# Kernel tuning notes

Measured on AMD Instinct MI355X. Metric: run time of the kernel, lower is better.

The kernel has to match this reference:

```python
import jax, jax.numpy as jnp
import numpy as np

A, R = 180, 180  # numAngle, numRho
EPS = 1e-5


def _hough_seg_ids(H, W):
    # Deep Hough Transform binning (Hanqer/deep-hough-transform initTab):
    # irho = int(sqrt(H^2+W^2)+1)/(numRho-1); theta_k = k*pi/numAngle
    irho = int(np.sqrt(H * H + W * W) + 1) / float(R - 1)
    theta = np.arange(A) * (np.pi / A)
    tab_cos = np.cos(theta) / irho  # [A]
    tab_sin = np.sin(theta) / irho
    xs = np.arange(W) - W // 2  # x is width index
    ys = np.arange(H) - H // 2
    r = np.round(tab_cos[:, None, None] * xs[None, None, :]
                 + tab_sin[:, None, None] * ys[None, :, None]).astype(np.int64) + R // 2
    r = np.clip(r, 0, R - 1)
    return jnp.asarray(r.reshape(A, H * W))  # [A, H*W] rho-bin per (angle, pixel)


def _conv_bn_relu(x, w, b, g, beta, m, v, pad):
    y = jax.lax.conv_general_dilated(
        x, w, window_strides=(1, 1), padding=[(pad, pad), (pad, pad)],
        dimension_numbers=('NCHW', 'OIHW', 'NCHW'))
    y = y + b[None, :, None, None]
    scale = g / jnp.sqrt(v + EPS)
    y = (y - m[None, :, None, None]) * scale[None, :, None, None] + beta[None, :, None, None]
    return jax.nn.relu(y)


def _dht(f):
    # f: [N, C, H, W] -> accum [N, C, A, R]
    N, C, H, W = f.shape
    seg = _hough_seg_ids(H, W)  # [A, HW]
    ft = f.reshape(N, C, H * W).transpose(2, 0, 1).reshape(H * W, N * C)  # [HW, N*C]
    acc = jax.vmap(lambda s: jax.ops.segment_sum(ft, s, num_segments=R))(seg)  # [A, R, N*C]
    return acc.reshape(A, R, N, C).transpose(2, 3, 0, 1)  # [N, C, A, R]


def setup_inputs() -> dict:
    key = jax.random.key(0)
    ks = jax.random.split(key, 24)
    N, Ci, dim, H, W = 8, 256, 128, 128, 128
    inp = {
        'x': jax.random.normal(ks[0], (N, Ci, H, W), jnp.float32),
        'w1': jax.random.normal(ks[1], (dim, Ci, 1, 1), jnp.float32) * (1.0 / np.sqrt(Ci)),
        'b1': jax.random.normal(ks[2], (dim,), jnp.float32) * 0.01,
        'g1': jax.random.uniform(ks[3], (dim,), jnp.float32, 0.5, 1.5),
        'be1': jax.random.normal(ks[4], (dim,), jnp.float32) * 0.01,
        'm1': jax.random.normal(ks[5], (dim,), jnp.float32) * 0.1,
        'v1': jax.random.uniform(ks[6], (dim,), jnp.float32, 0.5, 1.5),
        'w2': jax.random.normal(ks[7], (dim, dim, 3, 3), jnp.float32) * (1.0 / np.sqrt(dim * 9)),
        'b2': jax.random.normal(ks[8], (dim,), jnp.float32) * 0.01,
        'g2': jax.random.uniform(ks[9], (dim,), jnp.float32, 0.5, 1.5),
        'be2': jax.random.normal(ks[10], (dim,), jnp.float32) * 0.01,
        'm2': jax.random.normal(ks[11], (dim,), jnp.float32) * 0.1,
        'v2': jax.random.uniform(ks[12], (dim,), jnp.float32, 0.5, 1.5),
        'w3': jax.random.normal(ks[13], (dim, dim, 3, 3), jnp.float32) * (1.0 / np.sqrt(dim * 9)),
        'b3': jax.random.normal(ks[14], (dim,), jnp.float32) * 0.01,
        'g3': jax.random.uniform(ks[15], (dim,), jnp.float32, 0.5, 1.5),
        'be3': jax.random.normal(ks[16], (dim,), jnp.float32) * 0.01,
        'm3': jax.random.normal(ks[17], (dim,), jnp.float32) * 0.1,
        'v3': jax.random.uniform(ks[18], (dim,), jnp.float32, 0.5, 1.5),
    }
    return inp


def reference(x, w1, b1, g1, be1, m1, v1,
              w2, b2, g2, be2, m2, v2,
              w3, b3, g3, be3, m3, v3):
    f = _conv_bn_relu(x, w1, b1, g1, be1, m1, v1, pad=0)   # 1x1 conv + BN + ReLU
    acc = _dht(f)                                           # [N, dim, A, R]
    y = _conv_bn_relu(acc, w2, b2, g2, be2, m2, v2, pad=1)  # 3x3 conv + BN + ReLU
    y = _conv_bn_relu(y, w3, b3, g3, be3, m3, v3, pad=1)
    return y
```

## Files before the change

### kernel.cpp

```cpp
#include <hip/hip_runtime.h>
#include <hip/hip_bf16.h>
#include <math.h>

#define NB 8
#define CI 256
#define CD 128
#define HH 128
#define WW 128
#define HW (HH*WW)
#define AANG 180
#define RRHO 180
#define PADD 182
#define M2 (AANG*RRHO)

typedef __attribute__((ext_vector_type(8))) short short8;
typedef __attribute__((ext_vector_type(8))) _Float16 half8;
typedef __attribute__((ext_vector_type(2))) _Float16 h2;
typedef __attribute__((ext_vector_type(4))) float floatx4;
typedef __attribute__((ext_vector_type(2))) float floatx2;

static __device__ __forceinline__ void async_cp16(const void* g, void* l) {
  __builtin_amdgcn_global_load_lds((const __attribute__((address_space(1))) unsigned int*)g,
                                   (__attribute__((address_space(3))) unsigned int*)l,
                                   16, 0, 0);
}

static __device__ __forceinline__ unsigned short f2bf(float f) {
  unsigned int u = __builtin_bit_cast(unsigned int, f);
  unsigned int r = (u + 0x7fffu + ((u >> 16) & 1u)) >> 16;
  return (unsigned short)r;
}

static __device__ __forceinline__ unsigned short f2h(float f) {
  return __builtin_bit_cast(unsigned short, (_Float16)f);
}

static __device__ __forceinline__ void acc2(float& aL, float& aH, unsigned int u,
                                            h2 eL, h2 eH) {
  h2 hv = __builtin_bit_cast(h2, u);
#if __has_builtin(__builtin_amdgcn_fdot2)
  aL = __builtin_amdgcn_fdot2(hv, eL, aL, false);
  aH = __builtin_amdgcn_fdot2(hv, eH, aH, false);
#else
  aL += (float)hv.x;
  aH += (float)hv.y;
#endif
}

static __device__ __forceinline__ void acc4(float* aL, float* aH, const uint4& v,
                                            h2 eL, h2 eH) {
  acc2(aL[0], aH[0], v.x, eL, eH);
  acc2(aL[1], aH[1], v.y, eL, eH);
  acc2(aL[2], aH[2], v.z, eL, eH);
  acc2(aL[3], aH[3], v.w, eL, eH);
}

__global__ void prep_kernel(const float* __restrict__ w1, const float* __restrict__ w2,
                            const float* __restrict__ w3,
                            const float* b1, const float* g1, const float* be1,
                            const float* m1, const float* v1,
                            const float* b2, const float* g2, const float* be2,
                            const float* m2, const float* v2,
                            const float* b3, const float* g3, const float* be3,
                            const float* m3, const float* v3,
                            unsigned short* __restrict__ wK1, unsigned short* __restrict__ wK2,
                            unsigned short* __restrict__ wK3,
                            float* __restrict__ sc, float* __restrict__ sh) {
  int idx = blockIdx.x * 256 + threadIdx.x;
  if (idx < 32768) {
    wK1[idx] = f2h(w1[idx]);
  } else if (idx < 32768 + 147456) {
    int i = idx - 32768;
    int co = i / 1152, k = i % 1152;
    int dydx = k >> 7, ci = k & 127;
    int dst = (((dydx*2 + (ci >> 6)) * 128 + co) * 64) + (ci & 63);
    wK2[dst] = f2bf(w2[(size_t)(co*128 + ci)*9 + dydx]);
  } else if (idx < 32768 + 2*147456) {
    int i = idx - 32768 - 147456;
    int co = i / 1152, k = i % 1152;
    int dydx = k >> 7, ci = k & 127;
    int dst = (((dydx*2 + (ci >> 6)) * 128 + co) * 64) + (ci & 63);
    wK3[dst] = f2bf(w3[(size_t)(co*128 + ci)*9 + dydx]);
  } else if (idx < 32768 + 2*147456 + 384) {
    int j = idx - 32768 - 2*147456;
    int c = j >> 7, co = j & 127;
    const float* b  = c==0?b1 :(c==1?b2 :b3);
    const float* g  = c==0?g1 :(c==1?g2 :g3);
    const float* be = c==0?be1:(c==1?be2:be3);
    const float* m  = c==0?m1 :(c==1?m2 :m3);
    const float* v  = c==0?v1 :(c==1?v2 :v3);
    float s = g[co] * rsqrtf(v[co] + 1e-5f);
    sc[c*128 + co] = s;
    sh[c*128 + co] = (b[co] - m[co]) * s + be[co];
  }
}

__global__ void hist_kernel(unsigned char* __restrict__ seg, unsigned int* __restrict__ offs) {
  int a = blockIdx.x, t = threadIdx.x;
  __shared__ unsigned int h[RRHO];
  if (t < RRHO) h[t] = 0;
  __syncthreads();
  double th = (double)a * (M_PI / 180.0);
  double Cc = cos(th) / (182.0 / 179.0);
  double Ss = sin(th) / (182.0 / 179.0);
  for (int p = t; p < HW; p += 256) {
    int x = (p & 127) - 64;
    int y = (p >> 7) - 64;
    int r = (int)rint(Cc * (double)x + Ss * (double)y) + 90;
    r = r < 0 ? 0 : (r > 179 ? 179 : r);
    seg[(size_t)a*HW + p] = (unsigned char)r;
    atomicAdd(&h[r], 1u);
  }
  __syncthreads();
  if (t == 0) {
    unsigned int run = 0;
    for (int r = 0; r < RRHO; ++r) { offs[a*192 + r] = run; run += h[r]; }
    offs[a*192 + RRHO] = run;
  }
}

__global__ void fill_kernel(const unsigned char* __restrict__ seg,
                            const unsigned int* __restrict__ offs,
                            unsigned short* __restrict__ lst16) {
  int a = blockIdx.x, t = threadIdx.x;
  __shared__ unsigned int pos[RRHO];
  if (t < RRHO) pos[t] = offs[a*192 + t];
  __syncthreads();
  int p0 = t * 64;
  for (int i = 0; i < 64; ++i) {
    int p = p0 + i;
    int r = seg[(size_t)a*HW + p];
    unsigned int ix = atomicAdd(&pos[r], 1u);
    lst16[(size_t)a*HW + ix] = (unsigned short)p;
  }
}

__global__ void zero_border(uint4* __restrict__ accP, uint4* __restrict__ y2P,
                            unsigned int* __restrict__ qcnt) {
  int idx = blockIdx.x * 256 + threadIdx.x;
  if (idx < 8) qcnt[idx] = 0;
  if (idx >= NB * PADD * PADD) return;
  int rc = idx % (PADD * PADD);
  int row = rc / PADD, col = rc % PADD;
  if (row != 0 && row != PADD-1 && col != 0 && col != PADD-1) return;
  uint4 z = {0u, 0u, 0u, 0u};
  size_t base = (size_t)idx * 16;
  #pragma unroll
  for (int i = 0; i < 16; ++i) { accP[base + i] = z; y2P[base + i] = z; }
}

__global__ __launch_bounds__(256) void conv1_kernel(
    const float* __restrict__ x, const unsigned short* __restrict__ wK,
    const float* __restrict__ sc, const float* __restrict__ sh,
    unsigned short* __restrict__ f) {
  __shared__ short Al[4*128*8];
  __shared__ short Bl[4*128*8];
  int t = threadIdx.x;
  int m0 = blockIdx.x * 128;
  int n = blockIdx.y;
  int lane = t & 63, wv = t >> 6, wm = wv & 1, wn = wv >> 1;
  int mloc = t & 127, octb = t >> 7;
  floatx4 acc[4][4];
  #pragma unroll
  for (int i = 0; i < 4; ++i)
    #pragma unroll
    for (int j = 0; j < 4; ++j) acc[i][j] = (floatx4){0.f, 0.f, 0.f, 0.f};
  const float* xn = x + (size_t)n * CI * HW;
  for (int kc = 0; kc < 8; ++kc) {
    if (kc) __syncthreads();
    #pragma unroll
    for (int j = 0; j < 2; ++j) {
      int oct = octb + 2*j;
      const float* src = xn + (size_t)(kc*32 + oct*8) * HW + m0 + mloc;
      float v[8];
      #pragma unroll
      for (int e = 0; e < 8; ++e) v[e] = src[(size_t)e * HW];
      uint4 pk;
      pk.x = __builtin_bit_cast(unsigned int, __builtin_amdgcn_cvt_pkrtz(v[0], v[1]));
      pk.y = __builtin_bit_cast(unsigned int, __builtin_amdgcn_cvt_pkrtz(v[2], v[3]));
      pk.z = __builtin_bit_cast(unsigned int, __builtin_amdgcn_cvt_pkrtz(v[4], v[5]));
      pk.w = __builtin_bit_cast(unsigned int, __builtin_amdgcn_cvt_pkrtz(v[6], v[7]));
      *reinterpret_cast<uint4*>(&Al[(size_t)(t + 256*j) * 8]) = pk;
    }
    #pragma unroll
    for (int j = 0; j < 2; ++j) {
      int oct = octb + 2*j;
      async_cp16(wK + (size_t)mloc * 256 + kc*32 + oct*8,
                 &Bl[(size_t)((t & 0xFFC0) + 256*j) * 8]);
    }
    __syncthreads();
    int q = lane >> 4, l15 = lane & 15;
    short8 af[4], bfr[4];
    #pragma unroll
    for (int i = 0; i < 4; ++i)
      af[i] = *reinterpret_cast<const short8*>(&Al[((q*128) + wm*64 + i*16 + l15) * 8]);
    #pragma unroll
    for (int j = 0; j < 4; ++j)
      bfr[j] = *reinterpret_cast<const short8*>(&Bl[((q*128) + wn*64 + j*16 + l15) * 8]);
    #pragma unroll
    for (int i = 0; i < 4; ++i)
      #pragma unroll
      for (int j = 0; j < 4; ++j)
        acc[i][j] = __builtin_amdgcn_mfma_f32_16x16x32_f16(
            __builtin_bit_cast(half8, af[i]), __builtin_bit_cast(half8, bfr[j]),
            acc[i][j], 0, 0, 0);
  }
  int q = lane >> 4, l15 = lane & 15;
  #pragma unroll
  for (int j = 0; j < 4; ++j) {
    int co = wn*64 + j*16 + l15;
    float s = sc[co], hb = sh[co];
    #pragma unroll
    for (int i = 0; i < 4; ++i) {
      #pragma unroll
      for (int rg = 0; rg < 4; ++rg) {
        int m = m0 + wm*64 + i*16 + q*4 + rg;
        float v = acc[i][j][rg] * s + hb;
        v = fmaxf(v, 0.f);
        f[((size_t)n * HW + m) * 128 + co] = f2h(v);
      }
    }
  }
}

__global__ __launch_bounds__(512, 8) void dht_kernel(
    const unsigned short* __restrict__ lst16, const unsigned int* __restrict__ offs,
    const unsigned int* __restrict__ f, unsigned int* __restrict__ accP,
    unsigned int* __restrict__ qcnt) {
  __shared__ unsigned short Ls[HW];
  __shared__ unsigned int Os[RRHO + 1];
  __shared__ int sWork;
  int t = threadIdx.x;
  if (t == 0) {
    unsigned int xcd;
    asm volatile("s_getreg_b32 %0, hwreg(HW_REG_XCC_ID, 0, 32)" : "=s"(xcd));
    xcd &= 7u;
    int work = 0;
    for (int k = 0; k < 8; ++k) {
      unsigned int q = (xcd + (unsigned int)k) & 7u;
      unsigned int tk = atomicAdd(&qcnt[q], 1u);
      if (tk < 360u) { work = (int)(q * 360u + tk); break; }
    }
    sWork = work;
  }
  __syncthreads();
  int work = sWork;
  int n = work / 360;
  int rem = work % 360;
  int h = rem / 180;
  int a = rem % 180;
  {
    const uint4* src = (const uint4*)(lst16 + (size_t)a * HW);
    uint4* dst = (uint4*)Ls;
    if (t < RRHO + 1) Os[t] = offs[a*192 + t];
    #pragma unroll
    for (int i = 0; i < 4; ++i) dst[t + 512*i] = src[t + 512*i];
  }
  __syncthreads();
  int w = t >> 6, lane = t & 63;
  int sub = lane >> 3;
  int co  = lane & 7;
  const char* fb = (const char*)(f + (size_t)n * HW * 64);
  unsigned int loff = (unsigned int)(h*32 + co*4) * 4u;
  const h2 eL = {(_Float16)1.0f, (_Float16)0.0f};
  const h2 eH = {(_Float16)0.0f, (_Float16)1.0f};
  for (int r = w; r < RRHO; r += 8) {
    int lo = (int)Os[r];
    int hi = (int)Os[r+1];
    float accL[4], accH[4];
    #pragma unroll
    for (int j = 0; j < 4; ++j) { accL[j] = 0.f; accH[j] = 0.f; }
    while (hi - lo >= 64) {
      unsigned int p0 = Ls[lo + sub];
      unsigned int p1 = Ls[lo + 8 + sub];
      unsigned int p2 = Ls[lo + 16 + sub];
      unsigned int p3 = Ls[lo + 24 + sub];
      unsigned int p4 = Ls[hi - 32 + sub];
      unsigned int p5 = Ls[hi - 24 + sub];
      unsigned int p6 = Ls[hi - 16 + sub];
      unsigned int p7 = Ls[hi - 8 + sub];
      uint4 v0 = *(const uint4*)(fb + ((p0 << 8) + loff));
      uint4 v1 = *(const uint4*)(fb + ((p1 << 8) + loff));
      uint4 v2 = *(const uint4*)(fb + ((p2 << 8) + loff));
      uint4 v3 = *(const uint4*)(fb + ((p3 << 8) + loff));
      uint4 v4 = *(const uint4*)(fb + ((p4 << 8) + loff));
      uint4 v5 = *(const uint4*)(fb + ((p5 << 8) + loff));
      uint4 v6 = *(const uint4*)(fb + ((p6 << 8) + loff));
      uint4 v7 = *(const uint4*)(fb + ((p7 << 8) + loff));
      acc4(accL, accH, v0, eL, eH); acc4(accL, accH, v1, eL, eH);
      acc4(accL, accH, v2, eL, eH); acc4(accL, accH, v3, eL, eH);
      acc4(accL, accH, v4, eL, eH); acc4(accL, accH, v5, eL, eH);
      acc4(accL, accH, v6, eL, eH); acc4(accL, accH, v7, eL, eH);
      lo += 32; hi -= 32;
    }
    for (; lo + 32 <= hi; lo += 32) {
      unsigned int p0 = Ls[lo + sub];
      unsigned int p1 = Ls[lo + 8 + sub];
      unsigned int p2 = Ls[lo + 16 + sub];
      unsigned int p3 = Ls[lo + 24 + sub];
      uint4 v0 = *(const uint4*)(fb + ((p0 << 8) + loff));
      uint4 v1 = *(const uint4*)(fb + ((p1 << 8) + loff));
      uint4 v2 = *(const uint4*)(fb + ((p2 << 8) + loff));
      uint4 v3 = *(const uint4*)(fb + ((p3 << 8) + loff));
      acc4(accL, accH, v0, eL, eH); acc4(accL, accH, v1, eL, eH);
      acc4(accL, accH, v2, eL, eH); acc4(accL, accH, v3, eL, eH);
    }
    for (; lo + 8 <= hi; lo += 8) {
      unsigned int p0 = Ls[lo + sub];
      uint4 v0 = *(const uint4*)(fb + ((p0 << 8) + loff));
      acc4(accL, accH, v0, eL, eH);
    }
    if (lo < hi) {
      int idx = lo + sub;
      int cl = idx < hi ? idx : (hi - 1);
      unsigned int p0 = Ls[cl];
      uint4 v0 = *(const uint4*)(fb + ((p0 << 8) + loff));
      if (idx >= hi) { v0.x = 0; v0.y = 0; v0.z = 0; v0.w = 0; }
      acc4(accL, accH, v0, eL, eH);
    }
    #pragma unroll
    for (int m = 8; m <= 32; m <<= 1) {
      #pragma unroll
      for (int j = 0; j < 4; ++j) {
        accL[j] += __shfl_xor(accL[j], m, 64);
        accH[j] += __shfl_xor(accH[j], m, 64);
      }
    }
    if (sub == 0) {
      uint4 out;
      out.x = (unsigned int)f2bf(accL[0]) | ((unsigned int)f2bf(accH[0]) << 16);
      out.y = (unsigned int)f2bf(accL[1]) | ((unsigned int)f2bf(accH[1]) << 16);
      out.z = (unsigned int)f2bf(accL[2]) | ((unsigned int)f2bf(accH[2]) << 16);
      out.w = (unsigned int)f2bf(accL[3]) | ((unsigned int)f2bf(accH[3]) << 16);
      size_t o = (((size_t)n*PADD + (a+1))*PADD + (r+1))*64 + h*32 + co*4;
      *(uint4*)(accP + o) = out;
    }
  }
}

template<int MODE>
__global__ __launch_bounds__(256) void conv3x3_kernel(
    const unsigned short* __restrict__ inP,
    const unsigned short* __restrict__ wKr,
    const float* __restrict__ sc, const float* __restrict__ sh,
    void* __restrict__ outp) {
  __shared__ short Al[2][128*64];
  __shared__ short Bl[2][128*64];
  int t = threadIdx.x;
  int m0 = blockIdx.x * 128;
  int n = blockIdx.y;
  int lane = t & 63, w = t >> 6, wm = w & 1, wn = w >> 1;
  floatx4 acc[4][4];
  #pragma unroll
  for (int i = 0; i < 4; ++i)
    #pragma unroll
    for (int j = 0; j < 4; ++j) acc[i][j] = (floatx4){0.f, 0.f, 0.f, 0.f};

  int srcOct = ((lane & 7) - (lane >> 3)) & 7;
  const unsigned short* rpA[4];
  unsigned int offB[4];
  #pragma unroll
  for (int i = 0; i < 4; ++i) {
    int row = w*32 + i*8 + (lane >> 3);
    int mg = m0 + row; if (mg > M2 - 1) mg = M2 - 1;
    int oa = mg / 180, orr = mg % 180;
    rpA[i] = inP + (((size_t)n*PADD + oa)*PADD + orr)*128 + srcOct*8;
    offB[i] = (unsigned int)(row*64 + srcOct*8);
  }

  auto stage = [&](int step, int b) {
    int dydx = step >> 1, cc2 = step & 1;
    int dy = (dydx * 11) >> 5, dx = dydx - dy*3;
    int doff = (dy*PADD + dx)*128 + cc2*64;
    #pragma unroll
    for (int i = 0; i < 4; ++i) {
      async_cp16(rpA[i] + doff, &Al[b][(size_t)((w*4 + i)*64 + lane) * 8]);
      async_cp16(wKr + (size_t)step*8192 + offB[i],
                 &Bl[b][(size_t)((w*4 + i)*64 + lane) * 8]);
    }
  };
  auto compute = [&](int b) {
    int q = lane >> 4, l15 = lane & 15;
    #pragma unroll
    for (int kk = 0; kk < 2; ++kk) {
      int o = kk*4 + q;
      int swz = ((o + l15) & 7) * 8;
      short8 rf[4], cf[4];
      #pragma unroll
      for (int i = 0; i < 4; ++i) {
        int addr = (wm*64 + i*16 + l15)*64 + swz;
        rf[i] = *reinterpret_cast<const short8*>(MODE == 1 ? &Al[b][addr] : &Bl[b][addr]);
      }
      #pragma unroll
      for (int j = 0; j < 4; ++j) {
        int addr = (wn*64 + j*16 + l15)*64 + swz;
        cf[j] = *reinterpret_cast<const short8*>(MODE == 1 ? &Bl[b][addr] : &Al[b][addr]);
      }
      #pragma unroll
      for (int i = 0; i < 4; ++i)
        #pragma unroll
        for (int j = 0; j < 4; ++j)
          acc[i][j] = __builtin_amdgcn_mfma_f32_16x16x32_bf16(rf[i], cf[j], acc[i][j], 0, 0, 0);
    }
  };

  stage(0, 0);
  #pragma unroll 1
  for (int s2 = 0; s2 < 9; ++s2) {
    stage(2*s2 + 1, 1);
    asm volatile("s_waitcnt vmcnt(8)" ::: "memory");
    __builtin_amdgcn_s_barrier();
    __builtin_amdgcn_sched_barrier(0);
    compute(0);
    asm volatile("s_waitcnt lgkmcnt(0)" ::: "memory");
    __builtin_amdgcn_s_barrier();
    if (s2 < 8) {
      stage(2*s2 + 2, 0);
      asm volatile("s_waitcnt vmcnt(8)" ::: "memory");
    } else {
      asm volatile("s_waitcnt vmcnt(0)" ::: "memory");
    }
    __builtin_amdgcn_s_barrier();
    __builtin_amdgcn_sched_barrier(0);
    compute(1);
    asm volatile("s_waitcnt lgkmcnt(0)" ::: "memory");
    __builtin_amdgcn_s_barrier();
  }

  int q = lane >> 4, l15 = lane & 15;
  if (MODE == 1) {
    unsigned short* out = (unsigned short*)outp;
    #pragma unroll
    for (int j = 0; j < 4; ++j) {
      int co = wn*64 + j*16 + l15;
      float s = sc[co], hb = sh[co];
      #pragma unroll
      for (int i = 0; i < 4; ++i) {
        #pragma unroll
        for (int rg = 0; rg < 4; ++rg) {
          int m = m0 + wm*64 + i*16 + q*4 + rg;
          if (m < M2) {
            float v = fmaxf(acc[i][j][rg] * s + hb, 0.f);
            int oa2 = m / 180, or2 = m % 180;
            out[(((size_t)n*PADD + oa2 + 1)*PADD + or2 + 1)*128 + co] = f2bf(v);
          }
        }
      }
    }
  } else {
    float* out = (float*)outp;
    #pragma unroll
    for (int i = 0; i < 4; ++i) {
      #pragma unroll
      for (int rg = 0; rg < 4; ++rg) {
        int co = wm*64 + i*16 + q*4 + rg;
        float s = sc[co], hb = sh[co];
        #pragma unroll
        for (int j = 0; j < 4; ++j) {
          int m = m0 + wn*64 + j*16 + l15;
          if (m < M2) {
            float v = fmaxf(acc[i][j][rg] * s + hb, 0.f);
            out[((size_t)n*128 + co)*M2 + m] = v;
          }
        }
      }
    }
  }
}

extern "C" void kernel_launch(void* const* d_in, const int* in_sizes, int n_in,
                              void* d_out, int out_size, void* d_ws, size_t ws_size,
                              hipStream_t stream) {
  const float* x  = (const float*)d_in[0];
  const float* w1 = (const float*)d_in[1];
  const float* b1 = (const float*)d_in[2];
  const float* g1 = (const float*)d_in[3];
  const float* be1= (const float*)d_in[4];
  const float* m1 = (const float*)d_in[5];
  const float* v1 = (const float*)d_in[6];
  const float* w2 = (const float*)d_in[7];
  const float* b2 = (const float*)d_in[8];
  const float* g2 = (const float*)d_in[9];
  const float* be2= (const float*)d_in[10];
  const float* m2 = (const float*)d_in[11];
  const float* v2 = (const float*)d_in[12];
  const float* w3 = (const float*)d_in[13];
  const float* b3 = (const float*)d_in[14];
  const float* g3 = (const float*)d_in[15];
  const float* be3= (const float*)d_in[16];
  const float* m3 = (const float*)d_in[17];
  const float* v3 = (const float*)d_in[18];

  size_t off = 0;
  char* ws = (char*)d_ws;
  auto alloc = [&](size_t sz) -> void* {
    void* p = ws + off;
    off = (off + sz + 255) & ~(size_t)255;
    return p;
  };
  unsigned short* fbuf = (unsigned short*)alloc((size_t)NB*HW*128*2);
  unsigned short* accP = (unsigned short*)alloc((size_t)NB*PADD*PADD*128*2);
  unsigned short* y2P  = (unsigned short*)alloc((size_t)NB*PADD*PADD*128*2);
  unsigned short* wK1  = (unsigned short*)alloc(32768*2);
  unsigned short* wK2  = (unsigned short*)alloc(147456*2);
  unsigned short* wK3  = (unsigned short*)alloc(147456*2);
  float* sc = (float*)alloc(384*4);
  float* sh = (float*)alloc(384*4);
  unsigned char* seg  = (unsigned char*)alloc((size_t)AANG*HW);
  unsigned int* offs  = (unsigned int*)alloc((size_t)AANG*192*4);
  unsigned short* lst16 = (unsigned short*)alloc((size_t)AANG*HW*2);
  unsigned int* qcnt  = (unsigned int*)alloc(8*4);

  prep_kernel<<<1282, 256, 0, stream>>>(w1, w2, w3,
      b1, g1, be1, m1, v1, b2, g2, be2, m2, v2, b3, g3, be3, m3, v3,
      wK1, wK2, wK3, sc, sh);
  hist_kernel<<<AANG, 256, 0, stream>>>(seg, offs);
  fill_kernel<<<AANG, 256, 0, stream>>>(seg, offs, lst16);
  zero_border<<<(NB*PADD*PADD + 255)/256, 256, 0, stream>>>((uint4*)accP, (uint4*)y2P, qcnt);
  conv1_kernel<<<dim3(HW/128, NB), 256, 0, stream>>>(x, wK1, sc, sh, fbuf);
  dht_kernel<<<NB*AANG*2, 512, 0, stream>>>(lst16, offs, (const unsigned int*)fbuf,
                                            (unsigned int*)accP, qcnt);
  conv3x3_kernel<1><<<dim3((M2 + 127)/128, NB), 256, 0, stream>>>(
      accP, wK2, sc + 128, sh + 128, y2P);
  conv3x3_kernel<2><<<dim3((M2 + 127)/128, NB), 256, 0, stream>>>(
      y2P, wK3, sc + 256, sh + 256, d_out);
}
```

Before: 790.8 us.

## Fuse hist/fill kernels and single-buffer conv3x3 with higher occupancy

Merges the Hough histogram and list-fill kernels into one kernel that keeps rho-bin ids in shared memory, removing a launch and the global seg buffer. The conv3x3 kernel drops its hand-scheduled double-buffered async pipeline in favour of a single LDS buffer with plain __syncthreads and a min-blocks launch bound of 4. This aims for more resident blocks to hide latency, but it gives up the explicit overlap of loads with MFMA compute.

```diff
diff --git a/kernel.cpp b/kernel.cpp
--- a/kernel.cpp
+++ b/kernel.cpp
@@ -95,9 +95,12 @@
   }
 }
 
-__global__ void hist_kernel(unsigned char* __restrict__ seg, unsigned int* __restrict__ offs) {
+__global__ void histfill_kernel(unsigned int* __restrict__ offs,
+                                unsigned short* __restrict__ lst16) {
   int a = blockIdx.x, t = threadIdx.x;
+  __shared__ unsigned char segL[HW];
   __shared__ unsigned int h[RRHO];
+  __shared__ unsigned int pos[RRHO];
   if (t < RRHO) h[t] = 0;
   __syncthreads();
   double th = (double)a * (M_PI / 180.0);
@@ -108,28 +111,24 @@
     int y = (p >> 7) - 64;
     int r = (int)rint(Cc * (double)x + Ss * (double)y) + 90;
     r = r < 0 ? 0 : (r > 179 ? 179 : r);
-    seg[(size_t)a*HW + p] = (unsigned char)r;
+    segL[p] = (unsigned char)r;
     atomicAdd(&h[r], 1u);
   }
   __syncthreads();
   if (t == 0) {
     unsigned int run = 0;
-    for (int r = 0; r < RRHO; ++r) { offs[a*192 + r] = run; run += h[r]; }
+    for (int r = 0; r < RRHO; ++r) {
+      pos[r] = run;
+      offs[a*192 + r] = run;
+      run += h[r];
+    }
     offs[a*192 + RRHO] = run;
   }
-}
-
-__global__ void fill_kernel(const unsigned char* __restrict__ seg,
-                            const unsigned int* __restrict__ offs,
-                            unsigned short* __restrict__ lst16) {
-  int a = blockIdx.x, t = threadIdx.x;
-  __shared__ unsigned int pos[RRHO];
-  if (t < RRHO) pos[t] = offs[a*192 + t];
   __syncthreads();
   int p0 = t * 64;
   for (int i = 0; i < 64; ++i) {
     int p = p0 + i;
-    int r = seg[(size_t)a*HW + p];
+    int r = segL[p];
     unsigned int ix = atomicAdd(&pos[r], 1u);
     lst16[(size_t)a*HW + ix] = (unsigned short)p;
   }
@@ -339,13 +338,13 @@
 }
 
 template<int MODE>
-__global__ __launch_bounds__(256) void conv3x3_kernel(
+__global__ __launch_bounds__(256, 4) void conv3x3_kernel(
     const unsigned short* __restrict__ inP,
     const unsigned short* __restrict__ wKr,
     const float* __restrict__ sc, const float* __restrict__ sh,
     void* __restrict__ outp) {
-  __shared__ short Al[2][128*64];
-  __shared__ short Bl[2][128*64];
+  __shared__ short Al[128*64];
+  __shared__ short Bl[128*64];
   int t = threadIdx.x;
   int m0 = blockIdx.x * 128;
   int n = blockIdx.y;
@@ -368,18 +367,18 @@
     offB[i] = (unsigned int)(row*64 + srcOct*8);
   }
 
-  auto stage = [&](int step, int b) {
+  for (int step = 0; step < 18; ++step) {
     int dydx = step >> 1, cc2 = step & 1;
     int dy = (dydx * 11) >> 5, dx = dydx - dy*3;
     int doff = (dy*PADD + dx)*128 + cc2*64;
+    if (step) __syncthreads();
     #pragma unroll
     for (int i = 0; i < 4; ++i) {
-      async_cp16(rpA[i] + doff, &Al[b][(size_t)((w*4 + i)*64 + lane) * 8]);
+      async_cp16(rpA[i] + doff, &Al[(size_t)((w*4 + i)*64 + lane) * 8]);
       async_cp16(wKr + (size_t)step*8192 + offB[i],
-                 &Bl[b][(size_t)((w*4 + i)*64 + lane) * 8]);
-    }
-  };
-  auto compute = [&](int b) {
+                 &Bl[(size_t)((w*4 + i)*64 + lane) * 8]);
+    }
+    __syncthreads();
     int q = lane >> 4, l15 = lane & 15;
     #pragma unroll
     for (int kk = 0; kk < 2; ++kk) {
@@ -389,12 +388,12 @@
       #pragma unroll
       for (int i = 0; i < 4; ++i) {
         int addr = (wm*64 + i*16 + l15)*64 + swz;
-        rf[i] = *reinterpret_cast<const short8*>(MODE == 1 ? &Al[b][addr] : &Bl[b][addr]);
+        rf[i] = *reinterpret_cast<const short8*>(MODE == 1 ? &Al[addr] : &Bl[addr]);
       }
       #pragma unroll
       for (int j = 0; j < 4; ++j) {
         int addr = (wn*64 + j*16 + l15)*64 + swz;
-        cf[j] = *reinterpret_cast<const short8*>(MODE == 1 ? &Bl[b][addr] : &Al[b][addr]);
+        cf[j] = *reinterpret_cast<const short8*>(MODE == 1 ? &Bl[addr] : &Al[addr]);
       }
       #pragma unroll
       for (int i = 0; i < 4; ++i)
@@ -402,31 +401,7 @@
         for (int j = 0; j < 4; ++j)
           acc[i][j] = __builtin_amdgcn_mfma_f32_16x16x32_bf16(rf[i], cf[j], acc[i][j], 0, 0, 0);
     }
-  };
-
-  stage(0, 0);
-  #pragma unroll 1
-  for (int s2 = 0; s2 < 9; ++s2) {
-    stage(2*s2 + 1, 1);
-    asm volatile("s_waitcnt vmcnt(8)" ::: "memory");
-    __builtin_amdgcn_s_barrier();
-    __builtin_amdgcn_sched_barrier(0);
-    compute(0);
-    asm volatile("s_waitcnt lgkmcnt(0)" ::: "memory");
-    __builtin_amdgcn_s_barrier();
-    if (s2 < 8) {
-      stage(2*s2 + 2, 0);
-      asm volatile("s_waitcnt vmcnt(8)" ::: "memory");
-    } else {
-      asm volatile("s_waitcnt vmcnt(0)" ::: "memory");
-    }
-    __builtin_amdgcn_s_barrier();
-    __builtin_amdgcn_sched_barrier(0);
-    compute(1);
-    asm volatile("s_waitcnt lgkmcnt(0)" ::: "memory");
-    __builtin_amdgcn_s_barrier();
-  }
-
+  }
   int q = lane >> 4, l15 = lane & 15;
   if (MODE == 1) {
     unsigned short* out = (unsigned short*)outp;
@@ -506,7 +481,6 @@
   unsigned short* wK3  = (unsigned short*)alloc(147456*2);
   float* sc = (float*)alloc(384*4);
   float* sh = (float*)alloc(384*4);
-  unsigned char* seg  = (unsigned char*)alloc((size_t)AANG*HW);
   unsigned int* offs  = (unsigned int*)alloc((size_t)AANG*192*4);
   unsigned short* lst16 = (unsigned short*)alloc((size_t)AANG*HW*2);
   unsigned int* qcnt  = (unsigned int*)alloc(8*4);
@@ -514,8 +488,7 @@
   prep_kernel<<<1282, 256, 0, stream>>>(w1, w2, w3,
       b1, g1, be1, m1, v1, b2, g2, be2, m2, v2, b3, g3, be3, m3, v3,
       wK1, wK2, wK3, sc, sh);
-  hist_kernel<<<AANG, 256, 0, stream>>>(seg, offs);
-  fill_kernel<<<AANG, 256, 0, stream>>>(seg, offs, lst16);
+  histfill_kernel<<<AANG, 256, 0, stream>>>(offs, lst16);
   zero_border<<<(NB*PADD*PADD + 255)/256, 256, 0, stream>>>((uint4*)accP, (uint4*)y2P, qcnt);
   conv1_kernel<<<dim3(HW/128, NB), 256, 0, stream>>>(x, wK1, sc, sh, fbuf);
   dht_kernel<<<NB*AANG*2, 512, 0, stream>>>(lst16, offs, (const unsigned int*)fbuf,
```

New measurement: 727.9 us. -8.0%, faster.
